# Kernel optimization log

Hardware: AMD Instinct MI355X
Metric: run time of the kernel (lower is better)

## Reference

```python
import jax, jax.numpy as jnp
import numpy as np

N = 256          # waveguide_dims
ITERN = 3        # iter_num
B = 8192         # batch
INDEX_END = 10   # MNIST classes
ALPHA = 0.1
G = 0.05 * np.pi
PHI_B = np.pi


def setup_inputs() -> dict:
    key = jax.random.key(0)
    k1, k2, k3, k4, k5 = jax.random.split(key, 5)
    two_pi = 2.0 * np.pi
    return {
        "x_real": jax.random.normal(k1, (B, N), dtype=jnp.float32),
        "x_imag": jax.random.normal(k2, (B, N), dtype=jnp.float32),
        "theta": jax.random.uniform(k3, (ITERN, N, N // 2), dtype=jnp.float32) * two_pi,
        "phi":   jax.random.uniform(k4, (ITERN, N, N // 2), dtype=jnp.float32) * two_pi,
        "gamma": jax.random.uniform(k5, (ITERN, N), dtype=jnp.float32) * two_pi,
    }


def _mzi_mesh(x, theta, phi, gamma):
    """Rectangular (Clements) MZI mesh: N layers of 2x2 rotations + output phases.
    x: [B, N] complex64; theta, phi: [N, N//2]; gamma: [N]."""
    L = theta.shape[0]
    shifts = jnp.arange(L) % 2                      # even/odd layer offset
    full = jnp.ones((N // 2,), dtype=bool)
    odd = full.at[-1].set(False)                    # wrap-around pair inactive on odd layers
    masks = jnp.where((shifts == 1)[:, None], odd[None, :], full[None, :])

    def step(xc, inp):
        th, ph, sh, mk = inp
        xr = jnp.roll(xc, -sh, axis=1).reshape(-1, N // 2, 2)
        x0, x1 = xr[..., 0], xr[..., 1]
        half = 0.5 * th
        s, c = jnp.sin(half), jnp.cos(half)
        pre = 1j * jnp.exp(1j * half)               # common MZI prefactor
        ep = jnp.exp(1j * ph)
        y0 = pre * (ep * s * x0 + c * x1)
        y1 = pre * (ep * c * x0 - s * x1)
        y0 = jnp.where(mk, y0, x0)
        y1 = jnp.where(mk, y1, x1)
        y = jnp.stack([y0, y1], axis=-1).reshape(-1, N)
        return jnp.roll(y, sh, axis=1), None

    x, _ = jax.lax.scan(step, x, (theta, phi, shifts, masks))
    return x * jnp.exp(1j * gamma)[None, :]


def _eo_nonlin(x):
    # phase = 0.5*g*|x|^2 + 0.5*phi_b ; out = sqrt(1-alpha)*cos(phase)*exp(-i phase)*x
    phase = 0.5 * G * (x.real ** 2 + x.imag ** 2) + 0.5 * PHI_B
    return np.float32(np.sqrt(1.0 - ALPHA)) * jnp.cos(phase) * jnp.exp(-1j * phase) * x


def reference(x_real, x_imag, theta, phi, gamma):
    x = x_real.astype(jnp.complex64) + 1j * x_imag.astype(jnp.complex64)
    for i in range(ITERN):
        x = _mzi_mesh(x, theta[i], phi[i], gamma[i])
        if i != ITERN - 1:
            x = _eo_nonlin(x)
    intensity = x.real ** 2 + x.imag ** 2            # cnormsq
    norm = jnp.sqrt(jnp.sum(intensity ** 2, axis=1, keepdims=True))
    intensity = intensity / jnp.maximum(norm, 1e-12)  # F.normalize(dim=1)
    return intensity[:, :INDEX_END]
```

## Files before the change

kernel.cpp:

```cpp
#include <hip/hip_runtime.h>
#include <math.h>

#define NWG 256
#define NPAIR 128
#define NITER 3
#define NBATCH 8192
#define KDIM 512
#define MSZ (512*512)

typedef __attribute__((ext_vector_type(8))) short short8;
typedef __attribute__((ext_vector_type(4))) float floatx4;

static __device__ __forceinline__ unsigned short f2bf(float f) {
    unsigned int u = __float_as_uint(f);
    unsigned int r = (u + 0x7fffu + ((u >> 16) & 1u)) >> 16;
    return (unsigned short)r;
}
static __device__ __forceinline__ float bf2f(unsigned short h) {
    return __uint_as_float(((unsigned int)h) << 16);
}
static __device__ __forceinline__ void bsplit(float v, unsigned short &h, unsigned short &l) {
    h = f2bf(v);
    l = f2bf(v - bf2f(h));
}
static __device__ __forceinline__ void async16(const void* g, void* l) {
    __builtin_amdgcn_global_load_lds(
        (const __attribute__((address_space(1))) unsigned int*)g,
        (__attribute__((address_space(3))) unsigned int*)l, 16, 0, 0);
}

static __device__ __forceinline__ void apply2(
    float &x0r, float &x0i, float &x1r, float &x1i,
    const float4 a, const float4 b)
{
    float y0r = a.x*x0r - a.y*x0i + a.z*x1r - a.w*x1i;
    float y0i = a.x*x0i + a.y*x0r + a.z*x1i + a.w*x1r;
    float y1r = b.x*x0r - b.y*x0i + b.z*x1r - b.w*x1i;
    float y1i = b.x*x0i + b.y*x0r + b.z*x1i + b.w*x1r;
    x0r = y0r; x0i = y0i; x1r = y1r; x1i = y1i;
}

__global__ void precompute_kernel(const float* __restrict__ theta,
                                  const float* __restrict__ phi,
                                  const float* __restrict__ gamma,
                                  float* __restrict__ coef,
                                  float* __restrict__ coefT,
                                  float* __restrict__ gexp)
{
    int idx = blockIdx.x * blockDim.x + threadIdx.x;
    if (idx < NITER * NWG * NPAIR) {
        float h  = 0.5f * theta[idx];
        float ph = phi[idx];
        float sh = sinf(h),  ch = cosf(h);
        float sp = sinf(ph), cp = cosf(ph);
        float pr = -sh, pii = ch;
        float qr = pr*cp - pii*sp;
        float qi = pr*sp + pii*cp;
        float Ar = qr*sh,  Ai = qi*sh;
        float Br = pr*ch,  Bi = pii*ch;
        float Cr = qr*ch,  Ci = qi*ch;
        float Dr = -pr*sh, Di = -pii*sh;
        float4* o = (float4*)coef + (size_t)idx * 2;
        o[0] = make_float4(Ar,Ai,Br,Bi);
        o[1] = make_float4(Cr,Ci,Dr,Di);
        float4* ot = (float4*)coefT + (size_t)idx * 2;
        ot[0] = make_float4(Ar,Ai,Cr,Ci);
        ot[1] = make_float4(Br,Bi,Dr,Di);
    }
    if (idx < NITER * NWG) {
        float g = gamma[idx];
        gexp[idx*2]   = cosf(g);
        gexp[idx*2+1] = sinf(g);
    }
}

__global__ void propagate_kernel(const float* __restrict__ coef,
                                 const float* __restrict__ coefT,
                                 const float* __restrict__ gexp,
                                 unsigned short* __restrict__ chunkH,
                                 unsigned short* __restrict__ chunkL)
{
    const int lane = threadIdx.x & 63;
    const int wv   = threadIdx.x >> 6;
    const int grp  = blockIdx.x >> 6;
    const int it   = grp >> 2, c = grp & 3;
    const int row  = (blockIdx.x & 63) * 4 + wv;
    const bool rev = (c & 1);
    const bool cj  = (c == 1) || (c == 2);

    float xr[4], xi[4];
    float gc = 1.0f, gs = 0.0f;
    if (c == 3) { gc = gexp[(it*NWG + row)*2]; gs = gexp[(it*NWG + row)*2 + 1]; }
#pragma unroll
    for (int e = 0; e < 4; ++e) {
        bool on = (4*lane + e) == row;
        xr[e] = on ? gc : 0.0f;
        xi[e] = on ? gs : 0.0f;
    }

    const float4* cb = (const float4*)(rev ? coefT : coef)
                     + ((size_t)(it*NWG + c*64) * NPAIR) * 2;
    int sp0 = rev ? 63 : 0;
    const float4* p = cb + ((size_t)sp0 * NPAIR + 2*lane) * 2;
    float4 c0a = p[0], c0b = p[1], c1a = p[2], c1b = p[3];

    for (int s = 0; s < 64; ++s) {
        int sn  = (s + 1 < 64) ? s + 1 : s;
        int spn = rev ? 63 - sn : sn;
        const float4* np = cb + ((size_t)spn * NPAIR + 2*lane) * 2;
        float4 n0a = np[0], n0b = np[1], n1a = np[2], n1b = np[3];

        int sp = rev ? 63 - s : s;
        if ((sp & 1) == 0) {
            apply2(xr[0], xi[0], xr[1], xi[1], c0a, c0b);
            apply2(xr[2], xi[2], xr[3], xi[3], c1a, c1b);
        } else {
            float tr = __shfl_down(xr[0], 1, 64);
            float ti = __shfl_down(xi[0], 1, 64);
            apply2(xr[1], xi[1], xr[2], xi[2], c0a, c0b);
            float x3r = xr[3], x3i = xi[3];
            float y3r = c1a.x*x3r - c1a.y*x3i + c1a.z*tr - c1a.w*ti;
            float y3i = c1a.x*x3i + c1a.y*x3r + c1a.z*ti + c1a.w*tr;
            float ynr = c1b.x*x3r - c1b.y*x3i + c1b.z*tr - c1b.w*ti;
            float yni = c1b.x*x3i + c1b.y*x3r + c1b.z*ti + c1b.w*tr;
            float rr = __shfl_up(ynr, 1, 64);
            float ri = __shfl_up(yni, 1, 64);
            if (lane != 63) { xr[3] = y3r; xi[3] = y3i; }
            if (lane != 0)  { xr[0] = rr;  xi[0] = ri; }
        }
        c0a = n0a; c0b = n0b; c1a = n1a; c1b = n1b;
    }

    unsigned short* bh = chunkH + (size_t)grp * MSZ;
    unsigned short* bl = chunkL + (size_t)grp * MSZ;
    ushort4 reH, reL, imH, imL, nimH, nimL;
    unsigned short h, l;
#pragma unroll
    for (int e = 0; e < 4; ++e) {
        bsplit(xr[e], h, l);  ((unsigned short*)&reH)[e]  = h; ((unsigned short*)&reL)[e]  = l;
        bsplit(xi[e], h, l);  ((unsigned short*)&imH)[e]  = h; ((unsigned short*)&imL)[e]  = l;
        bsplit(-xi[e], h, l); ((unsigned short*)&nimH)[e] = h; ((unsigned short*)&nimL)[e] = l;
    }
    ushort4 urH = cj ? imH : nimH, urL = cj ? imL : nimL;
    ushort4 llH = cj ? nimH : imH, llL = cj ? nimL : imL;
    *(ushort4*)(bh + (size_t)row*KDIM + 4*lane)             = reH;
    *(ushort4*)(bh + (size_t)row*KDIM + 256 + 4*lane)       = urH;
    *(ushort4*)(bh + (size_t)(row+256)*KDIM + 4*lane)       = llH;
    *(ushort4*)(bh + (size_t)(row+256)*KDIM + 256 + 4*lane) = reH;
    *(ushort4*)(bl + (size_t)row*KDIM + 4*lane)             = reL;
    *(ushort4*)(bl + (size_t)row*KDIM + 256 + 4*lane)       = urL;
    *(ushort4*)(bl + (size_t)(row+256)*KDIM + 4*lane)       = llL;
    *(ushort4*)(bl + (size_t)(row+256)*KDIM + 256 + 4*lane) = reL;
}

__global__ __launch_bounds__(256, 2) void compose_kernel(
    const unsigned short* __restrict__ srcH, const unsigned short* __restrict__ srcL,
    unsigned short* __restrict__ outH, unsigned short* __restrict__ outL,
    unsigned short* __restrict__ bmat, int mode)
{
    __shared__ unsigned short sAh[2048], sAl[2048], sBh[2048], sBl[2048];
    const int z = blockIdx.z;
    const unsigned short *Ah, *Al, *Bh, *Bl;
    if (mode == 0) {
        int it = z >> 1, wh = z & 1;
        int ai = it*4 + (wh ? 3 : 0), bi = it*4 + (wh ? 2 : 1);
        Ah = srcH + (size_t)ai*MSZ; Al = srcL + (size_t)ai*MSZ;
        Bh = srcH + (size_t)bi*MSZ; Bl = srcL + (size_t)bi*MSZ;
    } else {
        Ah = srcH + (size_t)(2*z+1)*MSZ; Al = srcL + (size_t)(2*z+1)*MSZ;
        Bh = srcH + (size_t)(2*z)*MSZ;   Bl = srcL + (size_t)(2*z)*MSZ;
    }
    const int tid = threadIdx.x, lane = tid & 63, wv = tid >> 6;
    const int quad = lane >> 4, l16 = lane & 15;
    const int m0 = blockIdx.x * 64, n0 = blockIdx.y * 64;
    const unsigned short* src = (wv==0)?Ah:(wv==1)?Al:(wv==2)?Bh:Bl;
    unsigned short* dst = (wv==0)?sAh:(wv==1)?sAl:(wv==2)?sBh:sBl;
    const int r0 = (wv < 2) ? m0 : n0;
    const int trowb = lane >> 2, tcol = (lane & 3) * 8;

    floatx4 acc[4] = {};
    for (int kt = 0; kt < KDIM; kt += 32) {
        __syncthreads();
#pragma unroll
        for (int i = 0; i < 4; ++i)
            async16(src + (size_t)(r0 + i*16 + trowb)*KDIM + kt + tcol,
                    dst + i*512 + lane*8);
        __syncthreads();
        short8 ah = *(const short8*)&sAh[(16*wv + l16)*32 + quad*8];
        short8 al = *(const short8*)&sAl[(16*wv + l16)*32 + quad*8];
#pragma unroll
        for (int ni = 0; ni < 4; ++ni) {
            short8 bh = *(const short8*)&sBh[(16*ni + l16)*32 + quad*8];
            short8 bl = *(const short8*)&sBl[(16*ni + l16)*32 + quad*8];
            acc[ni] = __builtin_amdgcn_mfma_f32_16x16x32_bf16(ah, bh, acc[ni], 0,0,0);
            acc[ni] = __builtin_amdgcn_mfma_f32_16x16x32_bf16(ah, bl, acc[ni], 0,0,0);
            acc[ni] = __builtin_amdgcn_mfma_f32_16x16x32_bf16(al, bh, acc[ni], 0,0,0);
        }
    }
#pragma unroll
    for (int ni = 0; ni < 4; ++ni)
#pragma unroll
        for (int rg = 0; rg < 4; ++rg) {
            int r = m0 + 16*wv + quad*4 + rg;
            int cc = n0 + 16*ni + l16;
            float v = acc[ni][rg];
            if (mode == 0) {
                float vs = (((z & 1) == 0) && ((r >= 256) != (cc >= 256))) ? -v : v;
                unsigned short h, l; bsplit(vs, h, l);
                outH[(size_t)z*MSZ + (size_t)r*KDIM + cc] = h;
                outL[(size_t)z*MSZ + (size_t)r*KDIM + cc] = l;
            } else {
                bmat[(size_t)z*MSZ + (size_t)r*KDIM + cc] = f2bf(v);
            }
        }
}

__global__ void convert_kernel(const float* __restrict__ xre,
                               const float* __restrict__ xim,
                               unsigned short* __restrict__ xb)
{
    int idx = blockIdx.x * 256 + threadIdx.x;
    int b = idx >> 8, j = idx & 255;
    xb[(size_t)b * KDIM + j]       = f2bf(xre[idx]);
    xb[(size_t)b * KDIM + 256 + j] = f2bf(xim[idx]);
}

__global__ __launch_bounds__(256, 2) void gemm_kernel(
    const unsigned short* __restrict__ A, const unsigned short* __restrict__ Bm,
    int mode, unsigned short* __restrict__ xout, float* __restrict__ Iout)
{
    __shared__ unsigned short sA[64*32];
    __shared__ unsigned short sB[128*32];
    const int tid = threadIdx.x, lane = tid & 63, wv = tid >> 6;
    const int quad = lane >> 4, l16 = lane & 15;
    const int m0 = blockIdx.x * 64, n0 = blockIdx.y * 64;
    const int trowb = lane >> 2, tcol = (lane & 3) * 8;

    floatx4 acc[8] = {};
    for (int kt = 0; kt < KDIM; kt += 32) {
        __syncthreads();
        async16(A + (size_t)(m0 + 16*wv + trowb)*KDIM + kt + tcol,
                &sA[wv*512 + lane*8]);
#pragma unroll
        for (int j = 0; j < 2; ++j) {
            int trow = 32*wv + 16*j + trowb;
            int grow = (trow < 64) ? (n0 + trow) : (n0 + trow + 192);
            async16(Bm + (size_t)grow*KDIM + kt + tcol,
                    &sB[(32*wv + 16*j)*32 + lane*8]);
        }
        __syncthreads();
        short8 a = *(const short8*)&sA[(16*wv + l16)*32 + quad*8];
#pragma unroll
        for (int ni = 0; ni < 8; ++ni) {
            short8 b = *(const short8*)&sB[(16*ni + l16)*32 + quad*8];
            acc[ni] = __builtin_amdgcn_mfma_f32_16x16x32_bf16(a, b, acc[ni], 0,0,0);
        }
    }
#pragma unroll
    for (int ni = 0; ni < 4; ++ni)
#pragma unroll
        for (int rg = 0; rg < 4; ++rg) {
            int row = m0 + 16*wv + quad*4 + rg;
            int cc  = n0 + 16*ni + l16;
            float yr = acc[ni][rg], yi = acc[ni+4][rg];
            if (mode == 2) {
                Iout[(size_t)row*256 + cc] = yr*yr + yi*yi;
            } else {
                float I = yr*yr + yi*yi;
                float phase = 0.078539816339744831f * I + 1.5707963267948966f;
                float sp, cp; __sincosf(phase, &sp, &cp);
                float f = 0.94868329805051381f * cp;
                xout[(size_t)row*KDIM + cc]       = f2bf(f*(cp*yr + sp*yi));
                xout[(size_t)row*KDIM + cc + 256] = f2bf(f*(cp*yi - sp*yr));
            }
        }
}

__global__ void final_kernel(const float* __restrict__ Ibuf,
                             float* __restrict__ out)
{
    const int lane = threadIdx.x & 63;
    const int wv   = threadIdx.x >> 6;
    const int row  = blockIdx.x * 4 + wv;
    float4 v = *(const float4*)(Ibuf + (size_t)row * 256 + 4*lane);
    float ss = v.x*v.x + v.y*v.y + v.z*v.z + v.w*v.w;
#pragma unroll
    for (int d = 1; d < 64; d <<= 1) ss += __shfl_xor(ss, d, 64);
    float inv = 1.0f / fmaxf(sqrtf(ss), 1e-12f);
    float* o = out + (size_t)row * 10;
    if (lane == 0)      { o[0]=v.x*inv; o[1]=v.y*inv; o[2]=v.z*inv; o[3]=v.w*inv; }
    else if (lane == 1) { o[4]=v.x*inv; o[5]=v.y*inv; o[6]=v.z*inv; o[7]=v.w*inv; }
    else if (lane == 2) { o[8]=v.x*inv; o[9]=v.y*inv; }
}

extern "C" void kernel_launch(void* const* d_in, const int* in_sizes, int n_in,
                              void* d_out, int out_size, void* d_ws, size_t ws_size,
                              hipStream_t stream)
{
    const float* x_real = (const float*)d_in[0];
    const float* x_imag = (const float*)d_in[1];
    const float* theta  = (const float*)d_in[2];
    const float* phi    = (const float*)d_in[3];
    const float* gamma  = (const float*)d_in[4];

    char* ws = (char*)d_ws;
    float* coef  = (float*)(ws + 0);
    float* coefT = (float*)(ws + 3145728);
    float* gexp  = (float*)(ws + 6291456);
    unsigned short* chunkH = (unsigned short*)(ws + 6297600);
    unsigned short* chunkL = (unsigned short*)(ws + 12589056);
    unsigned short* PH   = (unsigned short*)(ws + 0);
    unsigned short* PL   = (unsigned short*)(ws + 3145728);
    unsigned short* xbuf0 = (unsigned short*)(ws + 6297600);
    unsigned short* xbuf1 = (unsigned short*)(ws + 14686208);
    float* Ibuf = (float*)(ws + 14686208);
    unsigned short* Bmat = (unsigned short*)(ws + 23074816);

    precompute_kernel<<<(NITER*NWG*NPAIR + 255)/256, 256, 0, stream>>>(
        theta, phi, gamma, coef, coefT, gexp);

    propagate_kernel<<<768, 256, 0, stream>>>(coef, coefT, gexp, chunkH, chunkL);

    compose_kernel<<<dim3(8,8,6), 256, 0, stream>>>(chunkH, chunkL, PH, PL, Bmat, 0);
    compose_kernel<<<dim3(8,8,3), 256, 0, stream>>>(PH, PL, PH, PL, Bmat, 1);

    convert_kernel<<<NBATCH*NWG/256, 256, 0, stream>>>(x_real, x_imag, xbuf0);

    gemm_kernel<<<dim3(128,4), 256, 0, stream>>>(xbuf0, Bmat,           0, xbuf1, (float*)nullptr);
    gemm_kernel<<<dim3(128,4), 256, 0, stream>>>(xbuf1, Bmat + MSZ,     1, xbuf0, (float*)nullptr);
    gemm_kernel<<<dim3(128,4), 256, 0, stream>>>(xbuf0, Bmat + 2*MSZ,   2, (unsigned short*)nullptr, Ibuf);

    final_kernel<<<NBATCH/4, 256, 0, stream>>>(Ibuf, (float*)d_out);
}
```

Baseline: 191.7 us.

## Stage MZI coefficients through LDS with async multi-buffered prefetch in propagate

The propagate kernel now copies each pair of mesh layers' coefficients cooperatively into shared memory using async 16-byte loads, with a 4-deep ring buffer and explicit vmcnt waits plus barriers. The four waves in a block share one global fetch instead of each loading the same coefficients, and loads are issued several steps ahead to hide latency. A swizzled slot layout is meant to avoid LDS bank conflicts. This adds block-wide barriers every two layers and relies on a helper (async16) that does not appear in the visible hunks.

```diff
diff --git a/kernel.cpp b/kernel.cpp
--- a/kernel.cpp
+++ b/kernel.cpp
@@ -74,65 +74,10 @@
     }
 }
 
-__global__ void propagate_kernel(const float* __restrict__ coef,
-                                 const float* __restrict__ coefT,
-                                 const float* __restrict__ gexp,
-                                 unsigned short* __restrict__ chunkH,
-                                 unsigned short* __restrict__ chunkL)
-{
-    const int lane = threadIdx.x & 63;
-    const int wv   = threadIdx.x >> 6;
-    const int grp  = blockIdx.x >> 6;
-    const int it   = grp >> 2, c = grp & 3;
-    const int row  = (blockIdx.x & 63) * 4 + wv;
-    const bool rev = (c & 1);
-    const bool cj  = (c == 1) || (c == 2);
-
-    float xr[4], xi[4];
-    float gc = 1.0f, gs = 0.0f;
-    if (c == 3) { gc = gexp[(it*NWG + row)*2]; gs = gexp[(it*NWG + row)*2 + 1]; }
-#pragma unroll
-    for (int e = 0; e < 4; ++e) {
-        bool on = (4*lane + e) == row;
-        xr[e] = on ? gc : 0.0f;
-        xi[e] = on ? gs : 0.0f;
-    }
-
-    const float4* cb = (const float4*)(rev ? coefT : coef)
-                     + ((size_t)(it*NWG + c*64) * NPAIR) * 2;
-    int sp0 = rev ? 63 : 0;
-    const float4* p = cb + ((size_t)sp0 * NPAIR + 2*lane) * 2;
-    float4 c0a = p[0], c0b = p[1], c1a = p[2], c1b = p[3];
-
-    for (int s = 0; s < 64; ++s) {
-        int sn  = (s + 1 < 64) ? s + 1 : s;
-        int spn = rev ? 63 - sn : sn;
-        const float4* np = cb + ((size_t)spn * NPAIR + 2*lane) * 2;
-        float4 n0a = np[0], n0b = np[1], n1a = np[2], n1b = np[3];
-
-        int sp = rev ? 63 - s : s;
-        if ((sp & 1) == 0) {
-            apply2(xr[0], xi[0], xr[1], xi[1], c0a, c0b);
-            apply2(xr[2], xi[2], xr[3], xi[3], c1a, c1b);
-        } else {
-            float tr = __shfl_down(xr[0], 1, 64);
-            float ti = __shfl_down(xi[0], 1, 64);
-            apply2(xr[1], xi[1], xr[2], xi[2], c0a, c0b);
-            float x3r = xr[3], x3i = xi[3];
-            float y3r = c1a.x*x3r - c1a.y*x3i + c1a.z*tr - c1a.w*ti;
-            float y3i = c1a.x*x3i + c1a.y*x3r + c1a.z*ti + c1a.w*tr;
-            float ynr = c1b.x*x3r - c1b.y*x3i + c1b.z*tr - c1b.w*ti;
-            float yni = c1b.x*x3i + c1b.y*x3r + c1b.z*ti + c1b.w*tr;
-            float rr = __shfl_up(ynr, 1, 64);
-            float ri = __shfl_up(yni, 1, 64);
-            if (lane != 63) { xr[3] = y3r; xi[3] = y3i; }
-            if (lane != 0)  { xr[0] = rr;  xi[0] = ri; }
-        }
-        c0a = n0a; c0b = n0b; c1a = n1a; c1b = n1b;
-    }
-
-    unsigned short* bh = chunkH + (size_t)grp * MSZ;
-    unsigned short* bl = chunkL + (size_t)grp * MSZ;
+static __device__ __forceinline__ void store_row(
+    unsigned short* __restrict__ bh, unsigned short* __restrict__ bl,
+    int row, int lane, bool cj, const float xr[4], const float xi[4])
+{
     ushort4 reH, reL, imH, imL, nimH, nimL;
     unsigned short h, l;
 #pragma unroll
@@ -151,6 +96,93 @@
     *(ushort4*)(bl + (size_t)row*KDIM + 256 + 4*lane)       = urL;
     *(ushort4*)(bl + (size_t)(row+256)*KDIM + 4*lane)       = llL;
     *(ushort4*)(bl + (size_t)(row+256)*KDIM + 256 + 4*lane) = reL;
+}
+
+static __device__ __forceinline__ void layer_step(
+    const char* B, int lane, int sp, float xr[4], float xi[4])
+{
+    const int sw = (lane >> 1) & 3;
+    const float4 c0a = *(const float4*)(B + 16*(4*lane + (0 ^ sw)));
+    const float4 c0b = *(const float4*)(B + 16*(4*lane + (1 ^ sw)));
+    const float4 c1a = *(const float4*)(B + 16*(4*lane + (2 ^ sw)));
+    const float4 c1b = *(const float4*)(B + 16*(4*lane + (3 ^ sw)));
+    if ((sp & 1) == 0) {
+        apply2(xr[0], xi[0], xr[1], xi[1], c0a, c0b);
+        apply2(xr[2], xi[2], xr[3], xi[3], c1a, c1b);
+    } else {
+        float tr = __shfl_down(xr[0], 1, 64);
+        float ti = __shfl_down(xi[0], 1, 64);
+        apply2(xr[1], xi[1], xr[2], xi[2], c0a, c0b);
+        float x3r = xr[3], x3i = xi[3];
+        float y3r = c1a.x*x3r - c1a.y*x3i + c1a.z*tr - c1a.w*ti;
+        float y3i = c1a.x*x3i + c1a.y*x3r + c1a.z*ti + c1a.w*tr;
+        float ynr = c1b.x*x3r - c1b.y*x3i + c1b.z*tr - c1b.w*ti;
+        float yni = c1b.x*x3i + c1b.y*x3r + c1b.z*ti + c1b.w*tr;
+        float rr = __shfl_up(ynr, 1, 64);
+        float ri = __shfl_up(yni, 1, 64);
+        if (lane != 63) { xr[3] = y3r; xi[3] = y3i; }
+        if (lane != 0)  { xr[0] = rr;  xi[0] = ri; }
+    }
+}
+
+__global__ void propagate_kernel(const float* __restrict__ coef,
+                                 const float* __restrict__ coefT,
+                                 const float* __restrict__ gexp,
+                                 unsigned short* __restrict__ chunkH,
+                                 unsigned short* __restrict__ chunkL)
+{
+    __shared__ __align__(16) char smem[4 * 8192];
+
+    const int tid  = threadIdx.x;
+    const int lane = tid & 63;
+    const int wv   = tid >> 6;
+    const int grp  = blockIdx.x >> 6;
+    const int it   = grp >> 2, c = grp & 3;
+    const int row  = (blockIdx.x & 63) * 4 + wv;
+    const bool rev = (c & 1);
+    const bool cj  = (c == 1) || (c == 2);
+
+    float xr[4], xi[4];
+    float gc = 1.0f, gs = 0.0f;
+    if (c == 3) { gc = gexp[(it*NWG + row)*2]; gs = gexp[(it*NWG + row)*2 + 1]; }
+#pragma unroll
+    for (int e = 0; e < 4; ++e) {
+        bool on = (4*lane + e) == row;
+        xr[e] = on ? gc : 0.0f;
+        xi[e] = on ? gs : 0.0f;
+    }
+
+    const char* cbb = (const char*)(rev ? coefT : coef)
+                    + (size_t)(it*NWG + c*64) * (NPAIR * 32);
+    const int slot16 = (tid ^ ((tid >> 3) & 3)) * 16;
+
+    auto stage = [&](int m) {
+        int s0 = 2*m, s1 = 2*m + 1;
+        int r0 = rev ? 63 - s0 : s0;
+        int r1 = rev ? 63 - s1 : s1;
+        char* dst = smem + (m & 3) * 8192;
+        async16(cbb + (size_t)r0 * 4096 + slot16, dst +        tid * 16);
+        async16(cbb + (size_t)r1 * 4096 + slot16, dst + 4096 + tid * 16);
+    };
+
+    stage(0); stage(1); stage(2);
+
+    for (int m = 0; m < 32; ++m) {
+        if (m < 30)       asm volatile("s_waitcnt vmcnt(4)" ::: "memory");
+        else if (m == 30) asm volatile("s_waitcnt vmcnt(2)" ::: "memory");
+        else              asm volatile("s_waitcnt vmcnt(0)" ::: "memory");
+        __builtin_amdgcn_s_barrier();
+        asm volatile("" ::: "memory");
+        if (m < 29) stage(m + 3);
+        const char* B = smem + (m & 3) * 8192;
+        int s0 = 2*m, s1 = 2*m + 1;
+        layer_step(B,        lane, rev ? 63 - s0 : s0, xr, xi);
+        layer_step(B + 4096, lane, rev ? 63 - s1 : s1, xr, xi);
+    }
+
+    unsigned short* bh = chunkH + (size_t)grp * MSZ;
+    unsigned short* bl = chunkL + (size_t)grp * MSZ;
+    store_row(bh, bl, row, lane, cj, xr, xi);
 }
 
 __global__ __launch_bounds__(256, 2) void compose_kernel(
```

Result: faster. 181.0 us (-5.6%).
